# Optimization experiments

Hardware: AMD Instinct MI355X
Metric: run time of the kernel (lower is better)

Reference implementation:

```python
import jax, jax.numpy as jnp
import numpy as np

N = 100000   # nodes per ntype
R = 3        # relations
E = 320000   # edges per relation
HID = 128    # hidden_dim (GATConv in_feats)
H, D = 4, 32 # num_heads, out_dim  -> H*D = 128
HD = H * D


def setup_inputs() -> dict:
    key = jax.random.key(0)
    ks = jax.random.split(key, 16)
    s = lambda k, shp, sc=0.05: jax.random.normal(k, shp, jnp.float32) * sc
    return {
        "dst_feat": s(ks[0], (N, HID), 1.0),
        "src_feats": s(ks[1], (R, N, HID), 1.0),
        "src_idx": jax.random.randint(ks[2], (R, E), 0, N, jnp.int32),
        "dst_idx": jax.random.randint(ks[3], (R, E), 0, N, jnp.int32),
        "Wt_dst": s(ks[4], (HID, HID)),
        "bt_dst": jnp.zeros((HID,), jnp.float32),
        "Wt_src": s(ks[5], (R, HID, HID)),
        "bt_src": jnp.zeros((R, HID), jnp.float32),
        "Wg": s(ks[6], (R, HID, HD)),
        "attn_l": s(ks[7], (R, H, D)),
        "attn_r": s(ks[8], (R, H, D)),
        "bias_g": jnp.zeros((R, HD), jnp.float32),
        "W1": s(ks[9], (HD, 128)),
        "b1": jnp.zeros((128,), jnp.float32),
        "W2": s(ks[10], (128, 1)),
    }


def _gat_rel(Wg, al, ar, bg, src_f, dst_f, s_idx, d_idx):
    # DGL GATConv, bipartite (src, dst), shared fc, eval mode (no dropout)
    hs = (src_f @ Wg).reshape(N, H, D)      # [N,H,D]
    hd = (dst_f @ Wg).reshape(N, H, D)
    el = (hs * al).sum(-1)                   # [N,H]
    er = (hd * ar).sum(-1)
    e = jax.nn.leaky_relu(el[s_idx] + er[d_idx], 0.2)   # [E,H]
    m = jax.ops.segment_max(e, d_idx, num_segments=N)    # edge-softmax over in-edges
    m = jnp.where(jnp.isfinite(m), m, 0.0)
    ex = jnp.exp(e - m[d_idx])
    ssum = jax.ops.segment_sum(ex, d_idx, num_segments=N)
    alpha = ex / (ssum[d_idx] + 1e-9)                    # [E,H]
    rst = jax.ops.segment_sum(alpha[:, :, None] * hs[s_idx], d_idx, num_segments=N)
    rst = rst + bg.reshape(1, H, D)
    return jax.nn.elu(rst).reshape(N, HD)


def reference(dst_feat, src_feats, src_idx, dst_idx, Wt_dst, bt_dst, Wt_src, bt_src,
              Wg, attn_l, attn_r, bias_g, W1, b1, W2):
    # weight_T per-ntype input projection (dim != hidden*num_heads branch)
    dstT = dst_feat @ Wt_dst + bt_dst                              # [N,HID]
    srcT = jnp.einsum('rnf,rfh->rnh', src_feats, Wt_src) + bt_src[:, None, :]
    # per-relation GATConv, vmapped over relations
    z_r = jax.vmap(_gat_rel, in_axes=(0, 0, 0, 0, 0, None, 0, 0))(
        Wg, attn_l, attn_r, bias_g, srcT, dstT, src_idx, dst_idx)  # [R,N,HD]
    z_m = jnp.transpose(z_r, (1, 0, 2))                            # [N,R,HD]
    # semantic attention
    w = jnp.tanh(z_m @ W1 + b1) @ W2                               # [N,R,1]
    a = jax.nn.softmax(w.mean(axis=0), axis=0)                     # [R,1]
    z = (z_m * a[None]).sum(axis=1)                                # [N,HD]
    att_mp = a.squeeze(-1)                                         # [R]
    return z, att_mp
```

## Files before the change

kernel.cpp:

```cpp
#include <hip/hip_runtime.h>
#include <hip/hip_bf16.h>
#include <math.h>

#define N_NODES 100000
#define R_REL 3
#define E_EDGES 320000
#define HID 128
#define HD 128
#define NBLK 391
#define GBLK 782

static constexpr size_t OFF_EXCSR = 0;
static constexpr size_t OFF_WTS_T = 16000000;
static constexpr size_t OFF_WG_T  = 16098304;
static constexpr size_t OFF_W1_T  = 16196608;
static constexpr size_t OFF_MER   = 16229376;
static constexpr size_t OFF_CER   = 16235520;
static constexpr size_t OFF_PART  = 16235584;
static constexpr size_t OFF_B1    = 51200000;
static constexpr size_t OFF_B2    = 204800000;
static constexpr size_t OFF_EL    = 358400000;
static constexpr size_t OFF_ER    = 363200000;
static constexpr size_t OFF_CNT   = 368006144;
static constexpr size_t OFF_OFFS  = 369206144;
static constexpr size_t OFF_CUR   = 370406272;
static constexpr size_t OFF_BSUM  = 371606272;
static constexpr size_t OFF_BOFF  = 371611136;
static constexpr size_t OFF_CSR   = 371616000;
static constexpr size_t OFF_ABUF  = 375456000;

typedef __attribute__((ext_vector_type(8))) short short8;
typedef __attribute__((ext_vector_type(4))) float floatx4;

__device__ __forceinline__ unsigned f2bf(float f)
{
    unsigned u = __float_as_uint(f);
    return (u + 0x7FFFu + ((u >> 16) & 1u)) >> 16;
}

__device__ __forceinline__ float fast_tanh(float x)
{
    x = fminf(fmaxf(x, -15.0f), 15.0f);
    float e = __expf(2.0f * x);
    return (e - 1.0f) / (e + 1.0f);
}

__global__ void transpose_bf16(const float* __restrict__ src, unsigned short* __restrict__ dst)
{
    int mat = blockIdx.y;
    int idx = blockIdx.x * 256 + threadIdx.x;
    int n = idx >> 7, k = idx & 127;
    dst[(size_t)mat * 16384 + n * 128 + k] =
        (unsigned short)f2bf(src[(size_t)mat * 16384 + k * 128 + n]);
}

__global__ __launch_bounds__(512) void prep_er(const float* __restrict__ Wg,
                                               const float* __restrict__ attn_r,
                                               const float* __restrict__ Wt_dst,
                                               const float* __restrict__ bt_dst,
                                               float* __restrict__ M, float* __restrict__ cvec)
{
    const int r = blockIdx.x;
    const int t = threadIdx.x;
    const int f = t >> 2, h = t & 3;
    __shared__ float wr[128][4];
    float s = 0.0f;
#pragma unroll
    for (int d = 0; d < 32; ++d)
        s += Wg[(size_t)r * 16384 + f * 128 + h * 32 + d] * attn_r[r * 128 + h * 32 + d];
    wr[f][h] = s;
    __syncthreads();
    float m = 0.0f;
    for (int k = 0; k < 128; ++k) m += Wt_dst[f * 128 + k] * wr[k][h];
    M[((size_t)r * 128 + f) * 4 + h] = m;
    if (f == 0) {
        float c = 0.0f;
        for (int k = 0; k < 128; ++k) c += bt_dst[k] * wr[k][h];
        cvec[r * 4 + h] = c;
    }
}

__global__ __launch_bounds__(256) void er_direct(const float* __restrict__ dst_feat,
                                                 const float* __restrict__ M,
                                                 const float* __restrict__ cvec,
                                                 float* __restrict__ er)
{
    int n = blockIdx.x * 4 + (threadIdx.x >> 6);
    int lane = threadIdx.x & 63;
    float d0 = dst_feat[(size_t)n * 128 + lane];
    float d1 = dst_feat[(size_t)n * 128 + 64 + lane];
#pragma unroll
    for (int r = 0; r < R_REL; ++r) {
        float4 w0 = *(const float4*)(M + ((size_t)r * 128 + lane) * 4);
        float4 w1 = *(const float4*)(M + ((size_t)r * 128 + 64 + lane) * 4);
        float p0 = d0 * w0.x + d1 * w1.x;
        float p1 = d0 * w0.y + d1 * w1.y;
        float p2 = d0 * w0.z + d1 * w1.z;
        float p3 = d0 * w0.w + d1 * w1.w;
#pragma unroll
        for (int off = 32; off >= 1; off >>= 1) {
            p0 += __shfl_down(p0, off);
            p1 += __shfl_down(p1, off);
            p2 += __shfl_down(p2, off);
            p3 += __shfl_down(p3, off);
        }
        if (lane == 0) {
            float4 c4 = *(const float4*)(cvec + r * 4);
            float4 o = { p0 + c4.x, p1 + c4.y, p2 + c4.z, p3 + c4.w };
            *(float4*)(er + ((size_t)r * N_NODES + n) * 4) = o;
        }
    }
}

#define XPITCH 136
__global__ __launch_bounds__(512) void fused_src_kernel(
    const float* __restrict__ src_feats, const unsigned short* __restrict__ WtsT,
    const float* __restrict__ bt_src, const unsigned short* __restrict__ WgT,
    const float* __restrict__ attn_l, unsigned short* __restrict__ hs, float* __restrict__ el)
{
    __shared__ unsigned short Xs[128 * XPITCH];
    const int r = blockIdx.y;
    const int row0 = blockIdx.x * 128;
    const int t = threadIdx.x, wave = t >> 6, lane = t & 63;
    const int wm = wave >> 2, wc = wave & 3, lm = lane & 15, quad = lane >> 4;
    const float* A = src_feats + (size_t)r * N_NODES * 128;

#pragma unroll
    for (int i = 0; i < 8; ++i) {
        int item = t + i * 512;
        int m = item >> 5, kq = item & 31;
        int gr = row0 + m; gr = gr < N_NODES ? gr : N_NODES - 1;
        float4 v = *(const float4*)(A + (size_t)gr * 128 + kq * 4);
        uint2 u;
        u.x = f2bf(v.x) | (f2bf(v.y) << 16);
        u.y = f2bf(v.z) | (f2bf(v.w) << 16);
        *(uint2*)(&Xs[m * XPITCH + kq * 4]) = u;
    }
    __syncthreads();

    floatx4 acc[4][2];
#pragma unroll
    for (int i = 0; i < 4; ++i)
#pragma unroll
        for (int j = 0; j < 2; ++j) acc[i][j] = (floatx4){0.f, 0.f, 0.f, 0.f};

    const unsigned short* B1 = WtsT + r * 16384;
#pragma unroll
    for (int kc = 0; kc < 4; ++kc) {
        short8 bk[2];
#pragma unroll
        for (int nt = 0; nt < 2; ++nt)
            bk[nt] = *(const short8*)(B1 + (wc * 32 + nt * 16 + lm) * 128 + kc * 32 + quad * 8);
        short8 af[4];
#pragma unroll
        for (int mt = 0; mt < 4; ++mt)
            af[mt] = *(const short8*)(&Xs[(wm * 64 + mt * 16 + lm) * XPITCH + kc * 32 + quad * 8]);
#pragma unroll
        for (int mt = 0; mt < 4; ++mt)
#pragma unroll
            for (int nt = 0; nt < 2; ++nt)
                acc[mt][nt] = __builtin_amdgcn_mfma_f32_16x16x32_bf16(af[mt], bk[nt], acc[mt][nt], 0, 0, 0);
    }
    __syncthreads();

#pragma unroll
    for (int mt = 0; mt < 4; ++mt) {
#pragma unroll
        for (int nt = 0; nt < 2; ++nt) {
            const int col = wc * 32 + nt * 16 + lm;
            const float bv = bt_src[r * 128 + col];
#pragma unroll
            for (int rg = 0; rg < 4; ++rg) {
                unsigned mb = f2bf(acc[mt][nt][rg] + bv);
                unsigned pb = (unsigned)__shfl_xor((int)mb, 1);
                if ((lm & 1) == 0) {
                    int trow = wm * 64 + mt * 16 + quad * 4 + rg;
                    *(unsigned*)(&Xs[trow * XPITCH + col]) = mb | (pb << 16);
                }
            }
        }
    }
    __syncthreads();

#pragma unroll
    for (int i = 0; i < 4; ++i)
#pragma unroll
        for (int j = 0; j < 2; ++j) acc[i][j] = (floatx4){0.f, 0.f, 0.f, 0.f};

    const unsigned short* B2 = WgT + r * 16384;
#pragma unroll
    for (int kc = 0; kc < 4; ++kc) {
        short8 bk[2];
#pragma unroll
        for (int nt = 0; nt < 2; ++nt)
            bk[nt] = *(const short8*)(B2 + (wc * 32 + nt * 16 + lm) * 128 + kc * 32 + quad * 8);
        short8 af[4];
#pragma unroll
        for (int mt = 0; mt < 4; ++mt)
            af[mt] = *(const short8*)(&Xs[(wm * 64 + mt * 16 + lm) * XPITCH + kc * 32 + quad * 8]);
#pragma unroll
        for (int mt = 0; mt < 4; ++mt)
#pragma unroll
            for (int nt = 0; nt < 2; ++nt)
                acc[mt][nt] = __builtin_amdgcn_mfma_f32_16x16x32_bf16(af[mt], bk[nt], acc[mt][nt], 0, 0, 0);
    }

    const float* alr = attn_l + r * 128;
    unsigned short* hsr = hs + (size_t)r * N_NODES * 128;
    float* elr = el + (size_t)r * N_NODES * 4;
#pragma unroll
    for (int mt = 0; mt < 4; ++mt) {
        float e4[4] = {0.f, 0.f, 0.f, 0.f};
#pragma unroll
        for (int nt = 0; nt < 2; ++nt) {
            const int col = wc * 32 + nt * 16 + lm;
            const float al = alr[col];
#pragma unroll
            for (int rg = 0; rg < 4; ++rg) {
                int gr = row0 + wm * 64 + mt * 16 + quad * 4 + rg;
                float v = acc[mt][nt][rg];
                unsigned mb = f2bf(v);
                unsigned pb = (unsigned)__shfl_xor((int)mb, 1);
                if ((lm & 1) == 0 && gr < N_NODES)
                    *(unsigned*)(hsr + (size_t)gr * 128 + col) = mb | (pb << 16);
                e4[rg] += v * al;
            }
        }
#pragma unroll
        for (int rg = 0; rg < 4; ++rg) {
            float a = e4[rg];
            a += __shfl_down(a, 8);
            a += __shfl_down(a, 4);
            a += __shfl_down(a, 2);
            a += __shfl_down(a, 1);
            if (lm == 0) {
                int gr = row0 + wm * 64 + mt * 16 + quad * 4 + rg;
                if (gr < N_NODES) elr[(size_t)gr * 4 + wc] = a;
            }
        }
    }
}

__global__ __launch_bounds__(256) void fused_sem_kernel(
    const float* __restrict__ zr, const unsigned short* __restrict__ W1T,
    const float* __restrict__ b1, const float* __restrict__ W2,
    float* __restrict__ partials)
{
    __shared__ unsigned short Xs[128 * XPITCH];
    const int r = blockIdx.y;
    const int row0 = blockIdx.x * 128;
    const int t = threadIdx.x, wave = t >> 6, lane = t & 63;
    const int wm = wave >> 1, wn = wave & 1, lm = lane & 15, quad = lane >> 4;
    const float* A = zr + (size_t)r * N_NODES * 128;

#pragma unroll
    for (int i = 0; i < 16; ++i) {
        int item = t + i * 256;
        int m = item >> 5, kq = item & 31;
        int gr = row0 + m; gr = gr < N_NODES ? gr : N_NODES - 1;
        float4 v = *(const float4*)(A + (size_t)gr * 128 + kq * 4);
        uint2 u;
        u.x = f2bf(v.x) | (f2bf(v.y) << 16);
        u.y = f2bf(v.z) | (f2bf(v.w) << 16);
        *(uint2*)(&Xs[m * XPITCH + kq * 4]) = u;
    }
    short8 bfrag[4][4];
#pragma unroll
    for (int nt = 0; nt < 4; ++nt)
#pragma unroll
        for (int kc = 0; kc < 4; ++kc)
            bfrag[nt][kc] = *(const short8*)(W1T + (wn * 64 + nt * 16 + lm) * 128 + kc * 32 + quad * 8);
    __syncthreads();

    floatx4 acc[4][4];
#pragma unroll
    for (int i = 0; i < 4; ++i)
#pragma unroll
        for (int j = 0; j < 4; ++j) acc[i][j] = (floatx4){0.f, 0.f, 0.f, 0.f};
#pragma unroll
    for (int kc = 0; kc < 4; ++kc) {
        short8 af[4];
#pragma unroll
        for (int mt = 0; mt < 4; ++mt)
            af[mt] = *(const short8*)(&Xs[(wm * 64 + mt * 16 + lm) * XPITCH + kc * 32 + quad * 8]);
#pragma unroll
        for (int mt = 0; mt < 4; ++mt)
#pragma unroll
            for (int nt = 0; nt < 4; ++nt)
                acc[mt][nt] = __builtin_amdgcn_mfma_f32_16x16x32_bf16(af[mt], bfrag[nt][kc], acc[mt][nt], 0, 0, 0);
    }

    float s = 0.0f;
#pragma unroll
    for (int nt = 0; nt < 4; ++nt) {
        const int col = wn * 64 + nt * 16 + lm;
        const float w2v = W2[col];
        const float b1v = b1[col];
#pragma unroll
        for (int mt = 0; mt < 4; ++mt)
#pragma unroll
            for (int rg = 0; rg < 4; ++rg) {
                int gr = row0 + wm * 64 + mt * 16 + quad * 4 + rg;
                if (gr < N_NODES) s += fast_tanh(acc[mt][nt][rg] + b1v) * w2v;
            }
    }
#pragma unroll
    for (int off = 32; off >= 1; off >>= 1) s += __shfl_down(s, off);
    __shared__ float ws4[4];
    if (lane == 0) ws4[wave] = s;
    __syncthreads();
    if (t == 0) partials[r * GBLK + blockIdx.x] = ws4[0] + ws4[1] + ws4[2] + ws4[3];
}

__global__ void count_kernel(const int* __restrict__ dst_idx, int* __restrict__ counts)
{
    int tid = blockIdx.x * 256 + threadIdx.x;
    if (tid >= R_REL * E_EDGES) return;
    int r = tid / E_EDGES;
    atomicAdd(&counts[r * N_NODES + dst_idx[tid]], 1);
}

__global__ void blocksum_kernel(const int* __restrict__ counts, int* __restrict__ bsums)
{
    int r = blockIdx.y;
    int i = blockIdx.x * 256 + threadIdx.x;
    int v = (i < N_NODES) ? counts[r * N_NODES + i] : 0;
#pragma unroll
    for (int off = 32; off >= 1; off >>= 1) v += __shfl_down(v, off);
    __shared__ int wsum[4];
    int lane = threadIdx.x & 63, w = threadIdx.x >> 6;
    if (lane == 0) wsum[w] = v;
    __syncthreads();
    if (threadIdx.x == 0) bsums[r * NBLK + blockIdx.x] = wsum[0] + wsum[1] + wsum[2] + wsum[3];
}

__global__ void scan_bsums(const int* __restrict__ bsums, int* __restrict__ boffs,
                           int* __restrict__ offs)
{
    int r = blockIdx.x;
    if (threadIdx.x != 0) return;
    int run = 0;
    for (int b = 0; b < NBLK; ++b) { boffs[r * NBLK + b] = run; run += bsums[r * NBLK + b]; }
    offs[r * (N_NODES + 1) + N_NODES] = run;
}

__global__ void scan_final(const int* __restrict__ counts, const int* __restrict__ boffs,
                           int* __restrict__ offs, int* __restrict__ cursor)
{
    int r = blockIdx.y;
    int i = blockIdx.x * 256 + threadIdx.x;
    int t = threadIdx.x;
    int v = (i < N_NODES) ? counts[r * N_NODES + i] : 0;
    __shared__ int sd[256];
    sd[t] = v;
    __syncthreads();
    for (int off = 1; off < 256; off <<= 1) {
        int y = (t >= off) ? sd[t - off] : 0;
        __syncthreads();
        sd[t] += y;
        __syncthreads();
    }
    int excl = sd[t] - v + boffs[r * NBLK + blockIdx.x];
    if (i < N_NODES) {
        offs[r * (N_NODES + 1) + i] = excl;
        cursor[r * N_NODES + i] = excl;
    }
}

__global__ void scatter_ex(const int* __restrict__ src_idx, const int* __restrict__ dst_idx,
                           const float* __restrict__ el, const float* __restrict__ er,
                           int* __restrict__ cursor, int* __restrict__ csr_src,
                           float* __restrict__ ex_csr)
{
    int tid = blockIdx.x * 256 + threadIdx.x;
    if (tid >= R_REL * E_EDGES) return;
    int r = tid / E_EDGES;
    int s = src_idx[tid], d = dst_idx[tid];
    float4 a = *(const float4*)(el + ((size_t)r * N_NODES + s) * 4);
    float4 b = *(const float4*)(er + ((size_t)r * N_NODES + d) * 4);
    float e0 = a.x + b.x, e1 = a.y + b.y, e2 = a.z + b.z, e3 = a.w + b.w;
    e0 = e0 > 0.f ? e0 : 0.2f * e0;
    e1 = e1 > 0.f ? e1 : 0.2f * e1;
    e2 = e2 > 0.f ? e2 : 0.2f * e2;
    e3 = e3 > 0.f ? e3 : 0.2f * e3;
    float4 ex = { __expf(e0), __expf(e1), __expf(e2), __expf(e3) };
    int pos = atomicAdd(&cursor[r * N_NODES + d], 1);
    csr_src[(size_t)r * E_EDGES + pos] = s;
    *(float4*)(ex_csr + ((size_t)r * E_EDGES + pos) * 4) = ex;
}

__global__ __launch_bounds__(256) void agg_kernel(
    const float* __restrict__ ex_csr, const unsigned short* __restrict__ hs,
    const int* __restrict__ offs, const int* __restrict__ csr_src,
    const float* __restrict__ bias_g, float* __restrict__ zr)
{
    const int lane = threadIdx.x & 63;
    const int half = lane >> 5;
    const int sl = lane & 31;
    const int g = blockIdx.x * 8 + (threadIdx.x >> 6) * 2 + half;
    const int r = g / N_NODES, n = g - r * N_NODES;
    const int comp = sl >> 3;
    const int cc = sl * 4;

    const int beg = offs[r * (N_NODES + 1) + n];
    const int end = offs[r * (N_NODES + 1) + n + 1];
    const int*   srcs = csr_src + (size_t)r * E_EDGES;
    const float* exc  = ex_csr + (size_t)r * E_EDGES * 4;
    const unsigned short* hsr = hs + (size_t)r * N_NODES * HD;
    const int L = lane & 32;

    float ss = 0.f, a0 = 0.f, a1 = 0.f, a2 = 0.f, a3 = 0.f;
    for (int base = beg; base < end; base += 32) {
        int j = base + sl;
        int jj = j < end ? j : base;
        int sv = srcs[jj];
        int cnt4 = (min(32, end - base) + 3) & ~3;
        for (int k = 0; k < cnt4; k += 4) {
            int b0 = base + k, b1 = b0 + 1, b2 = b0 + 2, b3 = b0 + 3;
            int s0 = __shfl(sv, L + k),     s1 = __shfl(sv, L + k + 1);
            int s2 = __shfl(sv, L + k + 2), s3 = __shfl(sv, L + k + 3);
            int j0 = b0 < end ? b0 : beg, j1 = b1 < end ? b1 : beg;
            int j2 = b2 < end ? b2 : beg, j3 = b3 < end ? b3 : beg;
            float e0 = exc[(size_t)j0 * 4 + comp];
            float e1 = exc[(size_t)j1 * 4 + comp];
            float e2 = exc[(size_t)j2 * 4 + comp];
            float e3 = exc[(size_t)j3 * 4 + comp];
            uint2 q0 = *(const uint2*)(hsr + (size_t)s0 * HD + cc);
            uint2 q1 = *(const uint2*)(hsr + (size_t)s1 * HD + cc);
            uint2 q2 = *(const uint2*)(hsr + (size_t)s2 * HD + cc);
            uint2 q3 = *(const uint2*)(hsr + (size_t)s3 * HD + cc);
            e0 = b0 < end ? e0 : 0.f;
            e1 = b1 < end ? e1 : 0.f;
            e2 = b2 < end ? e2 : 0.f;
            e3 = b3 < end ? e3 : 0.f;
            ss += e0 + e1 + e2 + e3;
            a0 += e0 * __uint_as_float(q0.x << 16) + e1 * __uint_as_float(q1.x << 16)
                + e2 * __uint_as_float(q2.x << 16) + e3 * __uint_as_float(q3.x << 16);
            a1 += e0 * __uint_as_float(q0.x & 0xffff0000u) + e1 * __uint_as_float(q1.x & 0xffff0000u)
                + e2 * __uint_as_float(q2.x & 0xffff0000u) + e3 * __uint_as_float(q3.x & 0xffff0000u);
            a2 += e0 * __uint_as_float(q0.y << 16) + e1 * __uint_as_float(q1.y << 16)
                + e2 * __uint_as_float(q2.y << 16) + e3 * __uint_as_float(q3.y << 16);
            a3 += e0 * __uint_as_float(q0.y & 0xffff0000u) + e1 * __uint_as_float(q1.y & 0xffff0000u)
                + e2 * __uint_as_float(q2.y & 0xffff0000u) + e3 * __uint_as_float(q3.y & 0xffff0000u);
        }
    }
    float inv = 1.0f / (ss + 1e-9f);
    float4 bg = *(const float4*)(bias_g + r * HD + cc);
    float r0 = a0 * inv + bg.x;
    float r1 = a1 * inv + bg.y;
    float r2 = a2 * inv + bg.z;
    float r3 = a3 * inv + bg.w;
    r0 = r0 > 0.0f ? r0 : (__expf(r0) - 1.0f);
    r1 = r1 > 0.0f ? r1 : (__expf(r1) - 1.0f);
    r2 = r2 > 0.0f ? r2 : (__expf(r2) - 1.0f);
    r3 = r3 > 0.0f ? r3 : (__expf(r3) - 1.0f);
    float4 o = { r0, r1, r2, r3 };
    *(float4*)(zr + (size_t)g * HD + cc) = o;
}

__global__ __launch_bounds__(256) void softmax_a(const float* __restrict__ partials,
                                                 float* __restrict__ a,
                                                 float* __restrict__ out)
{
    __shared__ float sm[3];
    const int t = threadIdx.x;
    if (t < 192) {
        const int r = t >> 6, lane = t & 63;
        float v = 0.0f;
        for (int i = lane; i < GBLK; i += 64) v += partials[r * GBLK + i];
#pragma unroll
        for (int off = 32; off >= 1; off >>= 1) v += __shfl_down(v, off);
        if (lane == 0) sm[r] = v;
    }
    __syncthreads();
    if (t == 0) {
        float w0 = sm[0] / (float)N_NODES;
        float w1 = sm[1] / (float)N_NODES;
        float w2 = sm[2] / (float)N_NODES;
        float m = fmaxf(w0, fmaxf(w1, w2));
        float e0 = __expf(w0 - m), e1 = __expf(w1 - m), e2 = __expf(w2 - m);
        float s = e0 + e1 + e2;
        a[0] = e0 / s; a[1] = e1 / s; a[2] = e2 / s;
        out[(size_t)N_NODES * HD + 0] = a[0];
        out[(size_t)N_NODES * HD + 1] = a[1];
        out[(size_t)N_NODES * HD + 2] = a[2];
    }
}

__global__ __launch_bounds__(256) void combine_kernel(const float* __restrict__ zr,
                                                      const float* __restrict__ a,
                                                      float* __restrict__ out)
{
    size_t i = (size_t)blockIdx.x * 256 + threadIdx.x;
    float a0 = a[0], a1 = a[1], a2 = a[2];
    const float4 v0 = ((const float4*)zr)[i];
    const float4 v1 = ((const float4*)(zr + (size_t)N_NODES * HD))[i];
    const float4 v2 = ((const float4*)(zr + 2 * (size_t)N_NODES * HD))[i];
    float4 o = { a0 * v0.x + a1 * v1.x + a2 * v2.x,
                 a0 * v0.y + a1 * v1.y + a2 * v2.y,
                 a0 * v0.z + a1 * v1.z + a2 * v2.z,
                 a0 * v0.w + a1 * v1.w + a2 * v2.w };
    ((float4*)out)[i] = o;
}

extern "C" void kernel_launch(void* const* d_in, const int* in_sizes, int n_in,
                              void* d_out, int out_size, void* d_ws, size_t ws_size,
                              hipStream_t stream)
{
    const float* dst_feat  = (const float*)d_in[0];
    const float* src_feats = (const float*)d_in[1];
    const int*   src_idx   = (const int*)d_in[2];
    const int*   dst_idx   = (const int*)d_in[3];
    const float* Wt_dst    = (const float*)d_in[4];
    const float* bt_dst    = (const float*)d_in[5];
    const float* Wt_src    = (const float*)d_in[6];
    const float* bt_src    = (const float*)d_in[7];
    const float* Wg        = (const float*)d_in[8];
    const float* attn_l    = (const float*)d_in[9];
    const float* attn_r    = (const float*)d_in[10];
    const float* bias_g    = (const float*)d_in[11];
    const float* W1        = (const float*)d_in[12];
    const float* b1        = (const float*)d_in[13];
    const float* W2        = (const float*)d_in[14];
    float* out = (float*)d_out;

    char* ws = (char*)d_ws;
    float*          ex_csr = (float*)(ws + OFF_EXCSR);
    unsigned short* WtsT   = (unsigned short*)(ws + OFF_WTS_T);
    unsigned short* WgT    = (unsigned short*)(ws + OFF_WG_T);
    unsigned short* W1T    = (unsigned short*)(ws + OFF_W1_T);
    float*          Mer    = (float*)(ws + OFF_MER);
    float*          cer    = (float*)(ws + OFF_CER);
    float*          parts  = (float*)(ws + OFF_PART);
    float*          zr     = (float*)(ws + OFF_B1);
    unsigned short* hs     = (unsigned short*)(ws + OFF_B2);
    float*          el     = (float*)(ws + OFF_EL);
    float*          er     = (float*)(ws + OFF_ER);
    int*            counts = (int*)(ws + OFF_CNT);
    int*            offs   = (int*)(ws + OFF_OFFS);
    int*            cursor = (int*)(ws + OFF_CUR);
    int*            bsums  = (int*)(ws + OFF_BSUM);
    int*            boffs  = (int*)(ws + OFF_BOFF);
    int*            csr    = (int*)(ws + OFF_CSR);
    float*          abuf   = (float*)(ws + OFF_ABUF);

    hipMemsetAsync(counts, 0, (size_t)R_REL * N_NODES * 4, stream);

    transpose_bf16<<<dim3(64, 3), 256, 0, stream>>>(Wt_src, WtsT);
    transpose_bf16<<<dim3(64, 3), 256, 0, stream>>>(Wg, WgT);
    transpose_bf16<<<dim3(64, 1), 256, 0, stream>>>(W1, W1T);
    prep_er<<<3, 512, 0, stream>>>(Wg, attn_r, Wt_dst, bt_dst, Mer, cer);

    fused_src_kernel<<<dim3(GBLK, 3), 512, 0, stream>>>(src_feats, WtsT, bt_src, WgT,
                                                        attn_l, hs, el);
    er_direct<<<25000, 256, 0, stream>>>(dst_feat, Mer, cer, er);

    count_kernel<<<3750, 256, 0, stream>>>(dst_idx, counts);
    blocksum_kernel<<<dim3(NBLK, 3), 256, 0, stream>>>(counts, bsums);
    scan_bsums<<<3, 64, 0, stream>>>(bsums, boffs, offs);
    scan_final<<<dim3(NBLK, 3), 256, 0, stream>>>(counts, boffs, offs, cursor);
    scatter_ex<<<3750, 256, 0, stream>>>(src_idx, dst_idx, el, er, cursor, csr, ex_csr);

    agg_kernel<<<37500, 256, 0, stream>>>(ex_csr, hs, offs, csr, bias_g, zr);

    fused_sem_kernel<<<dim3(GBLK, 3), 256, 0, stream>>>(zr, W1T, b1, W2, parts);
    softmax_a<<<1, 256, 0, stream>>>(parts, abuf, out);
    combine_kernel<<<12500, 256, 0, stream>>>(zr, abuf, out);
}
```

Baseline: 699.8 us.

## Loop relations inside fused_src_kernel and prefetch next relation's features into registers

```diff
diff --git a/kernel.cpp b/kernel.cpp
--- a/kernel.cpp
+++ b/kernel.cpp
@@ -118,124 +118,154 @@
     const float* __restrict__ bt_src, const unsigned short* __restrict__ WgT,
     const float* __restrict__ attn_l, unsigned short* __restrict__ hs, float* __restrict__ el)
 {
-    __shared__ unsigned short Xs[128 * XPITCH];
-    const int r = blockIdx.y;
+    __shared__ unsigned short X0[128 * XPITCH];
+    __shared__ unsigned short X1[128 * XPITCH];
     const int row0 = blockIdx.x * 128;
     const int t = threadIdx.x, wave = t >> 6, lane = t & 63;
     const int wm = wave >> 2, wc = wave & 3, lm = lane & 15, quad = lane >> 4;
-    const float* A = src_feats + (size_t)r * N_NODES * 128;
+
+    float4 L[8];
 
 #pragma unroll
     for (int i = 0; i < 8; ++i) {
         int item = t + i * 512;
         int m = item >> 5, kq = item & 31;
         int gr = row0 + m; gr = gr < N_NODES ? gr : N_NODES - 1;
-        float4 v = *(const float4*)(A + (size_t)gr * 128 + kq * 4);
+        L[i] = *(const float4*)(src_feats + (size_t)gr * 128 + kq * 4);
+    }
+#pragma unroll
+    for (int i = 0; i < 8; ++i) {
+        int item = t + i * 512;
+        int m = item >> 5, kq = item & 31;
         uint2 u;
-        u.x = f2bf(v.x) | (f2bf(v.y) << 16);
-        u.y = f2bf(v.z) | (f2bf(v.w) << 16);
-        *(uint2*)(&Xs[m * XPITCH + kq * 4]) = u;
-    }
-    __syncthreads();
-
-    floatx4 acc[4][2];
-#pragma unroll
-    for (int i = 0; i < 4; ++i)
-#pragma unroll
-        for (int j = 0; j < 2; ++j) acc[i][j] = (floatx4){0.f, 0.f, 0.f, 0.f};
-
-    const unsigned short* B1 = WtsT + r * 16384;
-#pragma unroll
-    for (int kc = 0; kc < 4; ++kc) {
-        short8 bk[2];
-#pragma unroll
-        for (int nt = 0; nt < 2; ++nt)
-            bk[nt] = *(const short8*)(B1 + (wc * 32 + nt * 16 + lm) * 128 + kc * 32 + quad * 8);
-        short8 af[4];
-#pragma unroll
-        for (int mt = 0; mt < 4; ++mt)
-            af[mt] = *(const short8*)(&Xs[(wm * 64 + mt * 16 + lm) * XPITCH + kc * 32 + quad * 8]);
-#pragma unroll
-        for (int mt = 0; mt < 4; ++mt)
+        u.x = f2bf(L[i].x) | (f2bf(L[i].y) << 16);
+        u.y = f2bf(L[i].z) | (f2bf(L[i].w) << 16);
+        *(uint2*)(&X0[m * XPITCH + kq * 4]) = u;
+    }
+    __syncthreads();
+
+    for (int r = 0; r < R_REL; ++r) {
+        if (r < R_REL - 1) {
+            const float* A = src_feats + (size_t)(r + 1) * N_NODES * 128;
+#pragma unroll
+            for (int i = 0; i < 8; ++i) {
+                int item = t + i * 512;
+                int m = item >> 5, kq = item & 31;
+                int gr = row0 + m; gr = gr < N_NODES ? gr : N_NODES - 1;
+                L[i] = *(const float4*)(A + (size_t)gr * 128 + kq * 4);
+            }
+        }
+
+        floatx4 acc[4][2];
+#pragma unroll
+        for (int i = 0; i < 4; ++i)
+#pragma unroll
+            for (int j = 0; j < 2; ++j) acc[i][j] = (floatx4){0.f, 0.f, 0.f, 0.f};
+
+        const unsigned short* B1 = WtsT + r * 16384;
+#pragma unroll
+        for (int kc = 0; kc < 4; ++kc) {
+            short8 bk[2];
 #pragma unroll
             for (int nt = 0; nt < 2; ++nt)
-                acc[mt][nt] = __builtin_amdgcn_mfma_f32_16x16x32_bf16(af[mt], bk[nt], acc[mt][nt], 0, 0, 0);
-    }
-    __syncthreads();
-
-#pragma unroll
-    for (int mt = 0; mt < 4; ++mt) {
-#pragma unroll
-        for (int nt = 0; nt < 2; ++nt) {
-            const int col = wc * 32 + nt * 16 + lm;
-            const float bv = bt_src[r * 128 + col];
-#pragma unroll
-            for (int rg = 0; rg < 4; ++rg) {
-                unsigned mb = f2bf(acc[mt][nt][rg] + bv);
-                unsigned pb = (unsigned)__shfl_xor((int)mb, 1);
-                if ((lm & 1) == 0) {
-                    int trow = wm * 64 + mt * 16 + quad * 4 + rg;
-                    *(unsigned*)(&Xs[trow * XPITCH + col]) = mb | (pb << 16);
+                bk[nt] = *(const short8*)(B1 + (wc * 32 + nt * 16 + lm) * 128 + kc * 32 + quad * 8);
+            short8 af[4];
+#pragma unroll
+            for (int mt = 0; mt < 4; ++mt)
+                af[mt] = *(const short8*)(&X0[(wm * 64 + mt * 16 + lm) * XPITCH + kc * 32 + quad * 8]);
+#pragma unroll
+            for (int mt = 0; mt < 4; ++mt)
+#pragma unroll
+                for (int nt = 0; nt < 2; ++nt)
+                    acc[mt][nt] = __builtin_amdgcn_mfma_f32_16x16x32_bf16(af[mt], bk[nt], acc[mt][nt], 0, 0, 0);
+        }
+        __syncthreads();
+
+#pragma unroll
+        for (int mt = 0; mt < 4; ++mt) {
+#pragma unroll
+            for (int nt = 0; nt < 2; ++nt) {
+                const int col = wc * 32 + nt * 16 + lm;
+                const float bv = bt_src[r * 128 + col];
+#pragma unroll
+                for (int rg = 0; rg < 4; ++rg) {
+                    unsigned mb = f2bf(acc[mt][nt][rg] + bv);
+                    unsigned pb = (unsigned)__shfl_xor((int)mb, 1);
+                    if ((lm & 1) == 0) {
+                        int trow = wm * 64 + mt * 16 + quad * 4 + rg;
+                        *(unsigned*)(&X1[trow * XPITCH + col]) = mb | (pb << 16);
+                    }
                 }
             }
         }
-    }
-    __syncthreads();
-
-#pragma unroll
-    for (int i = 0; i < 4; ++i)
-#pragma unroll
-        for (int j = 0; j < 2; ++j) acc[i][j] = (floatx4){0.f, 0.f, 0.f, 0.f};
-
-    const unsigned short* B2 = WgT + r * 16384;
-#pragma unroll
-    for (int kc = 0; kc < 4; ++kc) {
-        short8 bk[2];
-#pragma unroll
-        for (int nt = 0; nt < 2; ++nt)
-            bk[nt] = *(const short8*)(B2 + (wc * 32 + nt * 16 + lm) * 128 + kc * 32 + quad * 8);
-        short8 af[4];
-#pragma unroll
-        for (int mt = 0; mt < 4; ++mt)
-            af[mt] = *(const short8*)(&Xs[(wm * 64 + mt * 16 + lm) * XPITCH + kc * 32 + quad * 8]);
-#pragma unroll
-        for (int mt = 0; mt < 4; ++mt)
+        if (r < R_REL - 1) {
+#pragma unroll
+            for (int i = 0; i < 8; ++i) {
+                int item = t + i * 512;
+                int m = item >> 5, kq = item & 31;
+                uint2 u;
+                u.x = f2bf(L[i].x) | (f2bf(L[i].y) << 16);
+                u.y = f2bf(L[i].z) | (f2bf(L[i].w) << 16);
+                *(uint2*)(&X0[m * XPITCH + kq * 4]) = u;
+            }
+        }
+        __syncthreads();
+
+#pragma unroll
+        for (int i = 0; i < 4; ++i)
+#pragma unroll
+            for (int j = 0; j < 2; ++j) acc[i][j] = (floatx4){0.f, 0.f, 0.f, 0.f};
+
+        const unsigned short* B2 = WgT + r * 16384;
+#pragma unroll
+        for (int kc = 0; kc < 4; ++kc) {
+            short8 bk[2];
 #pragma unroll
             for (int nt = 0; nt < 2; ++nt)
-                acc[mt][nt] = __builtin_amdgcn_mfma_f32_16x16x32_bf16(af[mt], bk[nt], acc[mt][nt], 0, 0, 0);
-    }
-
-    const float* alr = attn_l + r * 128;
-    unsigned short* hsr = hs + (size_t)r * N_NODES * 128;
-    float* elr = el + (size_t)r * N_NODES * 4;
-#pragma unroll
-    for (int mt = 0; mt < 4; ++mt) {
-        float e4[4] = {0.f, 0.f, 0.f, 0.f};
-#pragma unroll
-        for (int nt = 0; nt < 2; ++nt) {
-            const int col = wc * 32 + nt * 16 + lm;
-            const float al = alr[col];
+                bk[nt] = *(const short8*)(B2 + (wc * 32 + nt * 16 + lm) * 128 + kc * 32 + quad * 8);
+            short8 af[4];
+#pragma unroll
+            for (int mt = 0; mt < 4; ++mt)
+                af[mt] = *(const short8*)(&X1[(wm * 64 + mt * 16 + lm) * XPITCH + kc * 32 + quad * 8]);
+#pragma unroll
+            for (int mt = 0; mt < 4; ++mt)
+#pragma unroll
+                for (int nt = 0; nt < 2; ++nt)
+                    acc[mt][nt] = __builtin_amdgcn_mfma_f32_16x16x32_bf16(af[mt], bk[nt], acc[mt][nt], 0, 0, 0);
+        }
+
+        const float* alr = attn_l + r * 128;
+        unsigned short* hsr = hs + (size_t)r * N_NODES * 128;
+        float* elr = el + (size_t)r * N_NODES * 4;
+#pragma unroll
+        for (int mt = 0; mt < 4; ++mt) {
+            float e4[4] = {0.f, 0.f, 0.f, 0.f};
+#pragma unroll
+            for (int nt = 0; nt < 2; ++nt) {
+                const int col = wc * 32 + nt * 16 + lm;
+                const float al = alr[col];
+#pragma unroll
+                for (int rg = 0; rg < 4; ++rg) {
+                    int gr = row0 + wm * 64 + mt * 16 + quad * 4 + rg;
+                    float v = acc[mt][nt][rg];
+                    unsigned mb = f2bf(v);
+                    unsigned pb = (unsigned)__shfl_xor((int)mb, 1);
+                    if ((lm & 1) == 0 && gr < N_NODES)
+                        *(unsigned*)(hsr + (size_t)gr * 128 + col) = mb | (pb << 16);
+                    e4[rg] += v * al;
+                }
+            }
 #pragma unroll
             for (int rg = 0; rg < 4; ++rg) {
-                int gr = row0 + wm * 64 + mt * 16 + quad * 4 + rg;
-                float v = acc[mt][nt][rg];
-                unsigned mb = f2bf(v);
-                unsigned pb = (unsigned)__shfl_xor((int)mb, 1);
-                if ((lm & 1) == 0 && gr < N_NODES)
-                    *(unsigned*)(hsr + (size_t)gr * 128 + col) = mb | (pb << 16);
-                e4[rg] += v * al;
-            }
-        }
-#pragma unroll
-        for (int rg = 0; rg < 4; ++rg) {
-            float a = e4[rg];
-            a += __shfl_down(a, 8);
-            a += __shfl_down(a, 4);
-            a += __shfl_down(a, 2);
-            a += __shfl_down(a, 1);
-            if (lm == 0) {
-                int gr = row0 + wm * 64 + mt * 16 + quad * 4 + rg;
-                if (gr < N_NODES) elr[(size_t)gr * 4 + wc] = a;
+                float a = e4[rg];
+                a += __shfl_down(a, 8);
+                a += __shfl_down(a, 4);
+                a += __shfl_down(a, 2);
+                a += __shfl_down(a, 1);
+                if (lm == 0) {
+                    int gr = row0 + wm * 64 + mt * 16 + quad * 4 + rg;
+                    if (gr < N_NODES) elr[(size_t)gr * 4 + wc] = a;
+                }
             }
         }
     }
@@ -551,8 +581,8 @@
     transpose_bf16<<<dim3(64, 1), 256, 0, stream>>>(W1, W1T);
     prep_er<<<3, 512, 0, stream>>>(Wg, attn_r, Wt_dst, bt_dst, Mer, cer);
 
-    fused_src_kernel<<<dim3(GBLK, 3), 512, 0, stream>>>(src_feats, WtsT, bt_src, WgT,
-                                                        attn_l, hs, el);
+    fused_src_kernel<<<dim3(GBLK), 512, 0, stream>>>(src_feats, WtsT, bt_src, WgT,
+                                                     attn_l, hs, el);
     er_direct<<<25000, 256, 0, stream>>>(dst_feat, Mer, cer, er);
 
     count_kernel<<<3750, 256, 0, stream>>>(dst_idx, counts);
```

Measured after the change: 766.1 us. +9.5%, slower.
